# Performance work log

Measured on AMD Instinct MI355X. Metric: run time of the kernel, lower is better.

Reference implementation:

```python
import jax, jax.numpy as jnp
import numpy as np

B, DIM, L = 4, 1024, 4096
N_CODES, CODE_DIM, H = 512, 256, 8
D = DIM // H  # head_dim = 128


def setup_inputs() -> dict:
    key = jax.random.key(0)
    k1, k2, k3, k4 = jax.random.split(key, 4)
    return {
        "x": jax.random.normal(k1, (B, DIM, L), dtype=jnp.float32),
        "codes": jax.random.normal(k2, (N_CODES, CODE_DIM), dtype=jnp.float32),
        "Wk": jax.random.normal(k3, (CODE_DIM, H, D), dtype=jnp.float32) * (CODE_DIM ** -0.5),
        "Wv": jax.random.normal(k4, (CODE_DIM, H, D), dtype=jnp.float32) * (CODE_DIM ** -0.5),
    }


def reference(x, codes, Wk, Wv):
    b, xdim, l = x.shape
    h, d = Wk.shape[1], Wk.shape[2]
    scale = d ** -0.5
    # b (h d) l -> b h l d
    q = scale * jnp.transpose(x.reshape(b, h, d, l), (0, 1, 3, 2))
    k = jnp.einsum('nc,chd->hnd', codes, Wk)  # [H, N, D]
    v = jnp.einsum('nc,chd->hnd', codes, Wv)  # [H, N, D]
    logits = jnp.einsum('bhld,hmd->bhlm', q, k)  # [B, H, L, N]
    idx = jnp.argmax(logits, axis=-1)  # [B, H, L] int
    # hard one-hot attention == direct gather from v
    h_ix = jnp.arange(h)[None, :, None]  # broadcast over B, L
    out = v[h_ix, idx]  # [B, H, L, D]
    out = jnp.transpose(out, (0, 1, 3, 2)).reshape(b, h * d, l)  # b (h d) l
    return out, idx
```

## Files before the change

kernel.cpp:

```cpp
#include <hip/hip_runtime.h>
#include <cstdint>

#define L_ 4096
#define NC_ 512
#define CD_ 256
#define H_ 8
#define D_ 128
#define B_ 4
#define SCALE 0.08838834764831845f
#define TAU 4.0e-3f

typedef _Float16 f16x8 __attribute__((ext_vector_type(8)));
typedef _Float16 f16x4 __attribute__((ext_vector_type(4)));
typedef float f32x16 __attribute__((ext_vector_type(16)));
typedef float f32x4 __attribute__((ext_vector_type(4)));

__global__ __launch_bounds__(256) void kv_pre(
    const float* __restrict__ codes, const float* __restrict__ Wk,
    const float* __restrict__ Wv, _Float16* __restrict__ K16f,
    float* __restrict__ K32, float* __restrict__ V)
{
    __shared__ float clds[16][260];
    const int t = threadIdx.x, h = blockIdx.y, n0 = blockIdx.x * 16;
    const int dz = blockIdx.z;
    {
        #pragma unroll
        for (int i = 0; i < 4; ++i) {
            int j = t + i*256;
            int row = j >> 6, c4 = j & 63;
            *(float4*)&clds[row][c4*4] =
                *(const float4*)(codes + (size_t)(n0 + row)*CD_ + c4*4);
        }
    }
    __syncthreads();
    const int nl = t >> 4;
    const int dq = t & 15;
    const int d0 = dz*64 + dq*4;
    const int n  = n0 + nl;
    const float4* wkp = (const float4*)Wk + h*32 + (d0 >> 2);
    const float4* wvp = (const float4*)Wv + h*32 + (d0 >> 2);

    float ak0=0,ak1=0,ak2=0,ak3=0, av0=0,av1=0,av2=0,av3=0;

    float4 wkb[4][4], wvb[4][4];
    #pragma unroll
    for (int s = 0; s < 4; ++s)
        #pragma unroll
        for (int u = 0; u < 4; ++u) {
            wkb[s][u] = wkp[(size_t)(s*4 + u)*256];
            wvb[s][u] = wvp[(size_t)(s*4 + u)*256];
        }

    for (int gg = 0; gg < 16; ++gg) {
        #pragma unroll
        for (int s = 0; s < 4; ++s) {
            const int g = gg*4 + s;
            float4 cv = *(const float4*)&clds[nl][g*4];
            #pragma unroll
            for (int u = 0; u < 4; ++u) {
                float cu = (u==0)?cv.x:(u==1)?cv.y:(u==2)?cv.z:cv.w;
                float4 wk = wkb[s][u];
                float4 wv = wvb[s][u];
                ak0 = fmaf(cu, wk.x, ak0); ak1 = fmaf(cu, wk.y, ak1);
                ak2 = fmaf(cu, wk.z, ak2); ak3 = fmaf(cu, wk.w, ak3);
                av0 = fmaf(cu, wv.x, av0); av1 = fmaf(cu, wv.y, av1);
                av2 = fmaf(cu, wv.z, av2); av3 = fmaf(cu, wv.w, av3);
            }
            if (g + 4 < 64) {
                #pragma unroll
                for (int u = 0; u < 4; ++u) {
                    wkb[s][u] = wkp[(size_t)((g+4)*4 + u)*256];
                    wvb[s][u] = wvp[(size_t)((g+4)*4 + u)*256];
                }
            }
        }
    }

    const size_t r32 = ((size_t)(h*NC_ + n))*D_ + d0;
    float4 sk; sk.x=ak0; sk.y=ak1; sk.z=ak2; sk.w=ak3;
    float4 sv; sv.x=av0; sv.y=av1; sv.z=av2; sv.w=av3;
    *(float4*)(K32 + r32) = sk;
    *(float4*)(V   + r32) = sv;
    f16x4 hk;
    hk[0]=(_Float16)(SCALE*ak0); hk[1]=(_Float16)(SCALE*ak1);
    hk[2]=(_Float16)(SCALE*ak2); hk[3]=(_Float16)(SCALE*ak3);
    const size_t a16 = ((size_t)((h*16 + (n>>5))*8 + (d0>>4))*64
                        + ((n&31) + ((d0>>3)&1)*32))*8 + (d0&7);
    *(f16x4*)(K16f + a16) = hk;
}

#define GLD_LDS16(GP, LP)                                                      \
  __builtin_amdgcn_global_load_lds(                                            \
      (const __attribute__((address_space(1))) void*)(GP),                     \
      (__attribute__((address_space(3))) void*)(LP), 16, 0, 0)

#define WAIT_VM0    asm volatile("s_waitcnt vmcnt(0)" ::: "memory")
#define WAIT_LGKM   asm volatile("s_waitcnt lgkmcnt(0)" ::: "memory")

#define QSTAGE(RD, QS)                                                         \
  _Pragma("unroll")                                                            \
  for (int i_ = 0; i_ < 4; ++i_) {                                             \
    const float* sp_ = xb + (size_t)((RD)*32 + i_*8 + (lane>>3))*L_            \
                          + l0w + (lane&7)*4;                                  \
    GLD_LDS16(sp_, (char*)(QS) + i_*1024);                                     \
  }

#define QREAD(RD, QS)                                                          \
  _Pragma("unroll")                                                            \
  for (int p_ = 0; p_ < 2; ++p_) {                                             \
    f16x8 tmp_;                                                                \
    _Pragma("unroll")                                                          \
    for (int j_ = 0; j_ < 8; ++j_)                                             \
      tmp_[j_] = (_Float16)((QS)[(p_*16 + hi*8 + j_)*32 + colL]);              \
    qf[(RD)*2 + p_] = tmp_;                                                    \
  }

#define KSTAGE(TI, DST)                                                        \
  GLD_LDS16(kh + ((size_t)(TI)*4096 + (wid*64 + lane)*8),                      \
            (DST) + (size_t)(wid*64)*8);                                       \
  GLD_LDS16(kh + ((size_t)(TI)*4096 + (256 + wid*64 + lane)*8),                \
            (DST) + (size_t)(256 + wid*64)*8);

__global__ __launch_bounds__(256, 4) void attn_main(
    const float* __restrict__ x, const _Float16* __restrict__ K16f,
    const float* __restrict__ K32, const float* __restrict__ V,
    float* __restrict__ out, float* __restrict__ idxf)
{
    __shared__ __align__(16) char smem[32768 + 2048];
    _Float16* bufA = (_Float16*)smem;
    _Float16* bufB = (_Float16*)(smem + 16384);
    float*    qbuf = (float*)(smem + 32768);

    const int t = threadIdx.x;
    const int wid = t >> 6, lane = t & 63;
    const int bid = blockIdx.x;
    const int h  = bid & 7;
    const int rr_ = bid >> 3;
    const int lx = rr_ & 31, b = rr_ >> 5;
    const int l0w = lx * 128 + wid * 32;

    const float* xb = x + ((size_t)(b*1024 + h*128)) * L_;
    const int colL = lane & 31;
    const int hi = lane >> 5;
    const int laneN4 = hi * 4;

    float* qs0 = (float*)(smem + wid * 8192);
    float* qs1 = (float*)(smem + wid * 8192 + 4096);
    f16x8 qf[8];
    QSTAGE(0, qs0)
    QSTAGE(1, qs1)
    WAIT_VM0;
    QREAD(0, qs0)
    QREAD(1, qs1)
    WAIT_LGKM;
    QSTAGE(2, qs0)
    QSTAGE(3, qs1)
    WAIT_VM0;
    QREAD(2, qs0)
    QREAD(3, qs1)
    __syncthreads();

    const _Float16* kh = K16f + ((size_t)h << 16);

    KSTAGE(0, bufA)
    KSTAGE(1, bufA + 4096)

    int nOr[16];
    #pragma unroll
    for (int r = 0; r < 16; ++r) nOr[r] = (r & 3) + ((r >> 2) << 3) + laneN4;
    float v1 = -INFINITY, v2 = -INFINITY, v3 = -INFINITY;

    __syncthreads();

    for (int m = 0; m < 8; ++m) {
        _Float16* cur = (m & 1) ? bufB : bufA;
        _Float16* nxt = (m & 1) ? bufA : bufB;
        if (m < 7) {
            KSTAGE(2*m + 2, nxt)
            KSTAGE(2*m + 3, nxt + 4096)
        }
        #pragma unroll
        for (int sub = 0; sub < 2; ++sub) {
            const _Float16* kt = cur + sub*4096;
            f32x16 acc;
            #pragma unroll
            for (int r = 0; r < 16; ++r) acc[r] = 0.f;
            #pragma unroll
            for (int ds = 0; ds < 8; ++ds) {
                f16x8 kf = *(const f16x8*)(kt + (size_t)(ds*64 + lane)*8);
                acc = __builtin_amdgcn_mfma_f32_32x32x16_f16(kf, qf[ds], acc, 0, 0, 0);
            }
            const int tb = (2*m + sub)*32;
            #pragma unroll
            for (int r = 0; r < 16; ++r) {
                int ki = (__float_as_int(acc[r]) & 0xFFFFFE00) | (tb + nOr[r]);
                float k = __int_as_float(ki);
                v3 = fmaxf(v3, fminf(fminf(v1, v2), k));
                float nv2 = __builtin_amdgcn_fmed3f(v1, v2, k);
                v1 = fmaxf(v1, k);
                v2 = nv2;
            }
        }
        __syncthreads();
    }

    float b1k = __shfl_xor(v1, 32);
    float b2k = __shfl_xor(v2, 32);
    float b3k = __shfl_xor(v3, 32);
    const float V1 = fmaxf(v1, b1k);
    const float c1 = fminf(v1, b1k);
    const float d1 = fmaxf(v2, b2k);
    const float V2 = fmaxf(c1, d1);
    const float V3 = __builtin_amdgcn_fmed3f(c1, d1, fmaxf(v3, b3k));
    const int I1 = __float_as_int(V1) & 511;
    const int I2 = __float_as_int(V2) & 511;
    int idx = I1;

    const bool cheap = (V1 - V2 < TAU) && (V1 - V3 >= TAU);
    const bool full  = (V1 - V3 < TAU);

    unsigned long long mc = __ballot(cheap) & 0xffffffffull;
    while (mc) {
        int src = (int)__builtin_ctzll(mc); mc &= mc - 1;
        int rl = l0w + src;
        int ra = __shfl(I1, src);
        int rb = __shfl(I2, src);
        int n = hi ? rb : ra;
        f32x4 kk = *(const f32x4*)(K32 + ((size_t)(h*NC_ + n))*D_ + colL*4);
        int dd = colL * 4;
        float q0 = SCALE * xb[(size_t)(dd+0)*L_ + rl];
        float q1 = SCALE * xb[(size_t)(dd+1)*L_ + rl];
        float q2 = SCALE * xb[(size_t)(dd+2)*L_ + rl];
        float q3 = SCALE * xb[(size_t)(dd+3)*L_ + rl];
        float p = q0 * kk[0];
        p = fmaf(q1, kk[1], p); p = fmaf(q2, kk[2], p); p = fmaf(q3, kk[3], p);
        #pragma unroll
        for (int m2 = 1; m2 < 32; m2 <<= 1) p += __shfl_xor(p, m2);
        float va = __shfl(p, 0);
        float vb = __shfl(p, 32);
        bool takeB = (vb > va) || (vb == va && rb < ra);
        int win = takeB ? rb : ra;
        if (lane == src) idx = win;
    }

    unsigned long long mf2 = __ballot(full) & 0xffffffffull;
    float* qb = qbuf + wid * 128;
    while (mf2) {
        int src = (int)__builtin_ctzll(mf2); mf2 &= mf2 - 1;
        int rl = l0w + src;
        qb[lane]      = SCALE * xb[(size_t)lane*L_ + rl];
        qb[lane + 64] = SCALE * xb[(size_t)(lane+64)*L_ + rl];
        __builtin_amdgcn_wave_barrier();
        WAIT_LGKM;
        float q0 = qb[colL*4+0], q1 = qb[colL*4+1], q2 = qb[colL*4+2], q3 = qb[colL*4+3];
        const f32x4* krow = (const f32x4*)(K32 + (size_t)h*NC_*D_);
        float bv = -INFINITY; int bn = 0;
        for (int i = 0; i < 256; i += 4) {
            #pragma unroll
            for (int u = 0; u < 4; ++u) {
                f32x4 kk = krow[(size_t)(i+u)*64 + lane];
                float p = q0 * kk[0];
                p = fmaf(q1, kk[1], p); p = fmaf(q2, kk[2], p); p = fmaf(q3, kk[3], p);
                #pragma unroll
                for (int m2 = 1; m2 < 32; m2 <<= 1) p += __shfl_xor(p, m2);
                const int n = 2*(i+u) + hi;
                if (p > bv) { bv = p; bn = n; }
            }
        }
        {
            float ov = __shfl_xor(bv, 32);
            int on = __shfl_xor(bn, 32);
            if (ov > bv || (ov == bv && on < bn)) { bv = ov; bn = on; }
        }
        if (lane == src) idx = bn;
        __builtin_amdgcn_wave_barrier();
    }
    idx = __shfl(idx, colL);

    const int myl = l0w + colL;
    if (!hi) idxf[((size_t)(b*H_ + h))*L_ + myl] = (float)idx;
    const f32x4* vrow = (const f32x4*)(V + ((size_t)(h*NC_ + idx))*D_);
    float* ob = out + ((size_t)(b*1024 + h*128 + hi*64))*L_ + myl;
    #pragma unroll
    for (int p = 0; p < 16; ++p) {
        f32x4 vv = vrow[hi*16 + p];
        ob[(size_t)(p*4+0)*L_] = vv[0];
        ob[(size_t)(p*4+1)*L_] = vv[1];
        ob[(size_t)(p*4+2)*L_] = vv[2];
        ob[(size_t)(p*4+3)*L_] = vv[3];
    }
}

extern "C" void kernel_launch(void* const* d_in, const int* in_sizes, int n_in,
                              void* d_out, int out_size, void* d_ws, size_t ws_size,
                              hipStream_t stream)
{
    const float* x     = (const float*)d_in[0];
    const float* codes = (const float*)d_in[1];
    const float* Wk    = (const float*)d_in[2];
    const float* Wv    = (const float*)d_in[3];

    float* out  = (float*)d_out;
    float* idxf = out + (size_t)B_ * H_ * D_ * L_;

    _Float16* K16f = (_Float16*)d_ws;
    float*    K32  = (float*)((char*)d_ws + (1u << 20));
    float*    Vf   = (float*)((char*)d_ws + (3u << 20));

    kv_pre<<<dim3(32, 8, 2), 256, 0, stream>>>(codes, Wk, Wv, K16f, K32, Vf);
    attn_main<<<dim3(1024), 256, 0, stream>>>(x, K16f, K32, Vf, out, idxf);
}
```

Measured before the change: 101.6 us.

## Process 64 query rows per wave to reuse each K fragment twice

Each wave now handles 64 L positions instead of 32, holding two Q fragment sets and issuing two MFMAs per K fragment read from LDS. This halves K staging traffic and the grid size per unit of work. The cost is more registers, so launch bounds drop to 2 blocks per CU, which lowers occupancy. kv_pre is now launched twice, which looks like an accidental duplicate that adds redundant work.

```diff
diff --git a/kernel.cpp b/kernel.cpp
--- a/kernel.cpp
+++ b/kernel.cpp
@@ -97,22 +97,22 @@
 #define WAIT_VM0    asm volatile("s_waitcnt vmcnt(0)" ::: "memory")
 #define WAIT_LGKM   asm volatile("s_waitcnt lgkmcnt(0)" ::: "memory")
 
-#define QSTAGE(RD, QS)                                                         \
+#define QST(DB, LB, QS)                                                        \
   _Pragma("unroll")                                                            \
   for (int i_ = 0; i_ < 4; ++i_) {                                             \
-    const float* sp_ = xb + (size_t)((RD)*32 + i_*8 + (lane>>3))*L_            \
-                          + l0w + (lane&7)*4;                                  \
+    const float* sp_ = xb + (size_t)((DB) + i_*8 + (lane>>3))*L_               \
+                          + (LB) + (lane&7)*4;                                 \
     GLD_LDS16(sp_, (char*)(QS) + i_*1024);                                     \
   }
 
-#define QREAD(RD, QS)                                                          \
+#define QRD(DB, QS, QF)                                                        \
   _Pragma("unroll")                                                            \
   for (int p_ = 0; p_ < 2; ++p_) {                                             \
     f16x8 tmp_;                                                                \
     _Pragma("unroll")                                                          \
     for (int j_ = 0; j_ < 8; ++j_)                                             \
       tmp_[j_] = (_Float16)((QS)[(p_*16 + hi*8 + j_)*32 + colL]);              \
-    qf[(RD)*2 + p_] = tmp_;                                                    \
+    QF[(DB)/16 + p_] = tmp_;                                                   \
   }
 
 #define KSTAGE(TI, DST)                                                        \
@@ -121,7 +121,14 @@
   GLD_LDS16(kh + ((size_t)(TI)*4096 + (256 + wid*64 + lane)*8),                \
             (DST) + (size_t)(256 + wid*64)*8);
 
-__global__ __launch_bounds__(256, 4) void attn_main(
+#define KEY3(KI, V1, V2, V3)                                                   \
+  { float k_ = __int_as_float(KI);                                             \
+    V3 = fmaxf(V3, fminf(fminf(V1, V2), k_));                                  \
+    float nv2_ = __builtin_amdgcn_fmed3f(V1, V2, k_);                          \
+    V1 = fmaxf(V1, k_);                                                        \
+    V2 = nv2_; }
+
+__global__ __launch_bounds__(256, 2) void attn_main(
     const float* __restrict__ x, const _Float16* __restrict__ K16f,
     const float* __restrict__ K32, const float* __restrict__ V,
     float* __restrict__ out, float* __restrict__ idxf)
@@ -136,8 +143,8 @@
     const int bid = blockIdx.x;
     const int h  = bid & 7;
     const int rr_ = bid >> 3;
-    const int lx = rr_ & 31, b = rr_ >> 5;
-    const int l0w = lx * 128 + wid * 32;
+    const int lx = rr_ & 15, b = rr_ >> 4;
+    const int l0w = lx * 256 + wid * 64;
 
     const float* xb = x + ((size_t)(b*1024 + h*128)) * L_;
     const int colL = lane & 31;
@@ -146,18 +153,30 @@
 
     float* qs0 = (float*)(smem + wid * 8192);
     float* qs1 = (float*)(smem + wid * 8192 + 4096);
-    f16x8 qf[8];
-    QSTAGE(0, qs0)
-    QSTAGE(1, qs1)
+    f16x8 qf0[8], qf1[8];
+    QST(0,  l0w,      qs0)
+    QST(0,  l0w + 32, qs1)
     WAIT_VM0;
-    QREAD(0, qs0)
-    QREAD(1, qs1)
+    QRD(0,  qs0, qf0)
+    QRD(0,  qs1, qf1)
     WAIT_LGKM;
-    QSTAGE(2, qs0)
-    QSTAGE(3, qs1)
+    QST(32, l0w,      qs0)
+    QST(32, l0w + 32, qs1)
     WAIT_VM0;
-    QREAD(2, qs0)
-    QREAD(3, qs1)
+    QRD(32, qs0, qf0)
+    QRD(32, qs1, qf1)
+    WAIT_LGKM;
+    QST(64, l0w,      qs0)
+    QST(64, l0w + 32, qs1)
+    WAIT_VM0;
+    QRD(64, qs0, qf0)
+    QRD(64, qs1, qf1)
+    WAIT_LGKM;
+    QST(96, l0w,      qs0)
+    QST(96, l0w + 32, qs1)
+    WAIT_VM0;
+    QRD(96, qs0, qf0)
+    QRD(96, qs1, qf1)
     __syncthreads();
 
     const _Float16* kh = K16f + ((size_t)h << 16);
@@ -168,7 +187,8 @@
     int nOr[16];
     #pragma unroll
     for (int r = 0; r < 16; ++r) nOr[r] = (r & 3) + ((r >> 2) << 3) + laneN4;
-    float v1 = -INFINITY, v2 = -INFINITY, v3 = -INFINITY;
+    float v1a = -INFINITY, v2a = -INFINITY, v3a = -INFINITY;
+    float v1b = -INFINITY, v2b = -INFINITY, v3b = -INFINITY;
 
     __syncthreads();
 
@@ -182,36 +202,48 @@
         #pragma unroll
         for (int sub = 0; sub < 2; ++sub) {
             const _Float16* kt = cur + sub*4096;
-            f32x16 acc;
-            #pragma unroll
-            for (int r = 0; r < 16; ++r) acc[r] = 0.f;
+            f32x16 a0, a1;
+            #pragma unroll
+            for (int r = 0; r < 16; ++r) { a0[r] = 0.f; a1[r] = 0.f; }
             #pragma unroll
             for (int ds = 0; ds < 8; ++ds) {
                 f16x8 kf = *(const f16x8*)(kt + (size_t)(ds*64 + lane)*8);
-                acc = __builtin_amdgcn_mfma_f32_32x32x16_f16(kf, qf[ds], acc, 0, 0, 0);
+                a0 = __builtin_amdgcn_mfma_f32_32x32x16_f16(kf, qf0[ds], a0, 0, 0, 0);
+                a1 = __builtin_amdgcn_mfma_f32_32x32x16_f16(kf, qf1[ds], a1, 0, 0, 0);
             }
             const int tb = (2*m + sub)*32;
             #pragma unroll
             for (int r = 0; r < 16; ++r) {
-                int ki = (__float_as_int(acc[r]) & 0xFFFFFE00) | (tb + nOr[r]);
-                float k = __int_as_float(ki);
-                v3 = fmaxf(v3, fminf(fminf(v1, v2), k));
-                float nv2 = __builtin_amdgcn_fmed3f(v1, v2, k);
-                v1 = fmaxf(v1, k);
-                v2 = nv2;
+                const int nn = tb + nOr[r];
+                int k0 = (__float_as_int(a0[r]) & 0xFFFFFE00) | nn;
+                int k1 = (__float_as_int(a1[r]) & 0xFFFFFE00) | nn;
+                KEY3(k0, v1a, v2a, v3a)
+                KEY3(k1, v1b, v2b, v3b)
             }
         }
         __syncthreads();
     }
 
-    float b1k = __shfl_xor(v1, 32);
-    float b2k = __shfl_xor(v2, 32);
-    float b3k = __shfl_xor(v3, 32);
-    const float V1 = fmaxf(v1, b1k);
-    const float c1 = fminf(v1, b1k);
-    const float d1 = fmaxf(v2, b2k);
-    const float V2 = fmaxf(c1, d1);
-    const float V3 = __builtin_amdgcn_fmed3f(c1, d1, fmaxf(v3, b3k));
+    float V1s[2], V2s[2], V3s[2];
+    {
+        float o1 = __shfl_xor(v1a, 32), o2 = __shfl_xor(v2a, 32), o3 = __shfl_xor(v3a, 32);
+        const float c1 = fminf(v1a, o1);
+        const float d1 = fmaxf(v2a, o2);
+        V1s[0] = fmaxf(v1a, o1);
+        V2s[0] = fmaxf(c1, d1);
+        V3s[0] = __builtin_amdgcn_fmed3f(c1, d1, fmaxf(v3a, o3));
+    }
+    {
+        float o1 = __shfl_xor(v1b, 32), o2 = __shfl_xor(v2b, 32), o3 = __shfl_xor(v3b, 32);
+        const float c1 = fminf(v1b, o1);
+        const float d1 = fmaxf(v2b, o2);
+        V1s[1] = fmaxf(v1b, o1);
+        V2s[1] = fmaxf(c1, d1);
+        V3s[1] = __builtin_amdgcn_fmed3f(c1, d1, fmaxf(v3b, o3));
+    }
+    const float V1 = hi ? V1s[1] : V1s[0];
+    const float V2 = hi ? V2s[1] : V2s[0];
+    const float V3 = hi ? V3s[1] : V3s[0];
     const int I1 = __float_as_int(V1) & 511;
     const int I2 = __float_as_int(V2) & 511;
     int idx = I1;
@@ -219,7 +251,7 @@
     const bool cheap = (V1 - V2 < TAU) && (V1 - V3 >= TAU);
     const bool full  = (V1 - V3 < TAU);
 
-    unsigned long long mc = __ballot(cheap) & 0xffffffffull;
+    unsigned long long mc = __ballot(cheap);
     while (mc) {
         int src = (int)__builtin_ctzll(mc); mc &= mc - 1;
         int rl = l0w + src;
@@ -243,7 +275,7 @@
         if (lane == src) idx = win;
     }
 
-    unsigned long long mf2 = __ballot(full) & 0xffffffffull;
+    unsigned long long mf2 = __ballot(full);
     float* qb = qbuf + wid * 128;
     while (mf2) {
         int src = (int)__builtin_ctzll(mf2); mf2 &= mf2 - 1;
@@ -275,15 +307,14 @@
         if (lane == src) idx = bn;
         __builtin_amdgcn_wave_barrier();
     }
-    idx = __shfl(idx, colL);
-
-    const int myl = l0w + colL;
-    if (!hi) idxf[((size_t)(b*H_ + h))*L_ + myl] = (float)idx;
+
+    const int myl = l0w + lane;
+    idxf[((size_t)(b*H_ + h))*L_ + myl] = (float)idx;
     const f32x4* vrow = (const f32x4*)(V + ((size_t)(h*NC_ + idx))*D_);
-    float* ob = out + ((size_t)(b*1024 + h*128 + hi*64))*L_ + myl;
+    float* ob = out + ((size_t)(b*1024 + h*128))*L_ + myl;
     #pragma unroll
-    for (int p = 0; p < 16; ++p) {
-        f32x4 vv = vrow[hi*16 + p];
+    for (int p = 0; p < 32; ++p) {
+        f32x4 vv = vrow[p];
         ob[(size_t)(p*4+0)*L_] = vv[0];
         ob[(size_t)(p*4+1)*L_] = vv[1];
         ob[(size_t)(p*4+2)*L_] = vv[2];
@@ -308,5 +339,6 @@
     float*    Vf   = (float*)((char*)d_ws + (3u << 20));
 
     kv_pre<<<dim3(32, 8, 2), 256, 0, stream>>>(codes, Wk, Wv, K16f, K32, Vf);
-    attn_main<<<dim3(1024), 256, 0, stream>>>(x, K16f, K32, Vf, out, idxf);
+    kv_pre<<<dim3(32, 8, 2), 256, 0, stream>>>(codes, Wk, Wv, K16f, K32, Vf);
+    attn_main<<<dim3(512), 256, 0, stream>>>(x, K16f, K32, Vf, out, idxf);
 }
```

After: 133.3 us. 31.2% more time.
